# Kernel optimization log

Hardware: AMD Instinct MI355X
Metric: run time of the kernel (lower is better)

Reference implementation:

```python
import jax, jax.numpy as jnp
import numpy as np
from jax import lax

B, C_IN, C_OUT, H, W, K, PAD = 4, 64, 64, 96, 96, 3, 1
K2 = K * K


def setup_inputs() -> dict:
    key = jax.random.key(0)
    k1, k2, k3, k4, k5 = jax.random.split(key, 5)
    x = jax.random.normal(k1, (B, C_IN, H, W), jnp.float32)
    offset = jax.random.normal(k2, (B, 2 * K2, H, W), jnp.float32)
    weight = jax.random.normal(k3, (C_OUT, C_IN, K, K), jnp.float32) * 0.05
    mask_weight = jax.random.normal(k4, (K2, C_IN, K, K), jnp.float32) * 0.05
    mask_bias = jax.random.normal(k5, (K2,), jnp.float32) * 0.05
    return {"x": x, "offset": offset, "weight": weight,
            "mask_weight": mask_weight, "mask_bias": mask_bias}


def _deform_conv2d(x, offset, weight, mask):
    # torchvision ordering: per kernel tap k, offset[:, 2k] is dy, offset[:, 2k+1] is dx
    off_y = offset[:, 0::2]  # [B, K2, H, W]
    off_x = offset[:, 1::2]
    ky, kx = jnp.meshgrid(jnp.arange(K), jnp.arange(K), indexing="ij")
    ky = ky.reshape(K2).astype(x.dtype)
    kx = kx.reshape(K2).astype(x.dtype)
    hh = jnp.arange(H, dtype=x.dtype)
    ww = jnp.arange(W, dtype=x.dtype)
    base_y = hh[None, :, None] - PAD + ky[:, None, None]   # [K2, H, 1]
    base_x = ww[None, None, :] - PAD + kx[:, None, None]   # [K2, 1, W]
    py = base_y[None] + off_y                               # [B, K2, H, W]
    px = base_x[None] + off_x

    y0 = jnp.floor(py)
    x0 = jnp.floor(px)
    wy = py - y0   # bilinear weights
    wx = px - x0
    y0i = y0.astype(jnp.int32)
    x0i = x0.astype(jnp.int32)

    x_flat = x.reshape(B, C_IN, H * W)

    def gather(yy, xx):
        valid = (yy >= 0) & (yy < H) & (xx >= 0) & (xx < W)
        idx = jnp.clip(yy, 0, H - 1) * W + jnp.clip(xx, 0, W - 1)  # [B,K2,H,W]
        idx_f = idx.reshape(B, -1)
        v = jax.vmap(lambda xf, i: xf[:, i])(x_flat, idx_f)  # [B, C, K2*H*W]
        v = v.reshape(B, C_IN, K2, H, W)
        return v * valid[:, None].astype(v.dtype)

    v00 = gather(y0i, x0i)
    v01 = gather(y0i, x0i + 1)
    v10 = gather(y0i + 1, x0i)
    v11 = gather(y0i + 1, x0i + 1)

    wy_ = wy[:, None]  # [B,1,K2,H,W]
    wx_ = wx[:, None]
    sampled = (v00 * (1 - wy_) * (1 - wx_) + v01 * (1 - wy_) * wx_
               + v10 * wy_ * (1 - wx_) + v11 * wy_ * wx_)
    sampled = sampled * mask[:, None]  # modulate by sigmoid mask

    w2 = weight.reshape(C_OUT, C_IN, K2)
    return jnp.einsum("bckhw,ock->bohw", sampled, w2)


def reference(x, offset, weight, mask_weight, mask_bias):
    mask_logits = lax.conv_general_dilated(
        x, mask_weight, window_strides=(1, 1), padding=[(PAD, PAD), (PAD, PAD)],
        dimension_numbers=("NCHW", "OIHW", "NCHW"))
    mask = jax.nn.sigmoid(mask_logits + mask_bias[None, :, None, None])
    return _deform_conv2d(x, offset, weight, mask)
```

## Files before the change

kernel.cpp:

```cpp
#include <hip/hip_runtime.h>
#include <math.h>

#define BB 4
#define CI 64
#define CO 64
#define HH 96
#define WW 96
#define HW (HH*WW)
#define K2 9
#define PADC 1

#define TW 4
#define TH 4
#define TPXT (TW*TH)
#define TBX (WW/TW)
#define TBY (HH/TH)
#define NTILB (TBX*TBY)
#define NTILES (BB*NTILB)
#define GRID 512

#define WR 13
#define WC 16
#define SREC 72
#define NSLOT (WR*WC)
#define STASKS (WR*32*4)

typedef __attribute__((ext_vector_type(8))) short short8;
typedef __attribute__((ext_vector_type(4))) float float4v;

#define WF_USHORTS (18*64*32)
#define MWF_USHORTS (18*16*32)

__device__ __forceinline__ float bf2f(short s) {
    return __uint_as_float(((unsigned int)(unsigned short)s) << 16);
}
__device__ __forceinline__ short f2bf(float f) {
    unsigned int u = __float_as_uint(f);
    u = (u + 0x7fffu + ((u >> 16) & 1u)) >> 16;
    return (short)u;
}

__device__ __forceinline__ void unswz(int tt, int* b, int* ty, int* tx) {
    int g = tt & 7, r = tt >> 3;
    *b = g & 3;
    int tile = (g >> 2) * 288 + r;
    *ty = tile / TBX; *tx = tile % TBX;
}

__global__ __launch_bounds__(256) void pack_kernel(const float* __restrict__ wgt,
                                                   const float* __restrict__ mw,
                                                   unsigned short* __restrict__ Wf,
                                                   unsigned short* __restrict__ MWf) {
    int i = blockIdx.x * 256 + threadIdx.x;
    if (i < WF_USHORTS) {
        int frag = i >> 11;
        int o = (i >> 5) & 63;
        int tt = i & 31;
        int k = frag >> 1, cc = frag & 1;
        int c = cc * 32 + tt;
        Wf[i] = (unsigned short)f2bf(wgt[o * 576 + c * 9 + k]);
    } else if (i < WF_USHORTS + MWF_USHORTS) {
        int e = i - WF_USHORTS;
        int frag = e >> 9;
        int m = (e >> 5) & 15;
        int tt = e & 31;
        int q = frag >> 1, cc = frag & 1;
        int c = cc * 32 + tt;
        MWf[e] = (m < 9) ? (unsigned short)f2bf(mw[m * 576 + c * 9 + q]) : 0;
    }
}

struct SmemT {
    unsigned short win[NSLOT * SREC];
    float mred[2][2][K2][TPXT];
    int   idx[K2][4][TPXT];
    float w[K2][4][TPXT];
};

template<int KB, int KE>
__device__ __forceinline__ void run_tiles(SmemT& sm, int t, int wv, int ch, int tg,
                                          const float* __restrict__ x,
                                          const float* __restrict__ off,
                                          const float* __restrict__ mbias,
                                          const unsigned short* __restrict__ Wf,
                                          const unsigned short* __restrict__ MWf,
                                          float* __restrict__ out, int bid) {
    constexpr int NK = KE - KB;
    int lane = t & 63;
    int n = lane & 15, quad = lane >> 4;
    float* part = (float*)sm.win;

    short8 wA[NK][4];
    short8 mA[NK];
    #pragma unroll
    for (int kk = 0; kk < NK; kk++) {
        int k = KB + kk;
        const unsigned short* wp = Wf + (size_t)((k * 2 + ch) * 64) * 32 + quad * 8;
        #pragma unroll
        for (int s = 0; s < 4; s++)
            wA[kk][s] = *(const short8*)(wp + (s * 16 + n) * 32);
        mA[kk] = *(const short8*)(MWf + ((size_t)((k * 2 + ch) * 16 + n)) * 32 + quad * 8);
    }

    int ly = n >> 2, lx = n & 3;
    int cbase_us = ch * 32 + quad * 8;

    for (int tt = bid; tt < NTILES; tt += GRID) {
        int b, ty, tx; unswz(tt, &b, &ty, &tx);
        int h0 = ty * TH, w0 = tx * TW;
        int wr0 = h0 - 4, wc0 = w0 - 4;
        const float* xb = x + (size_t)b * CI * HW;
        int h = h0 + ly, wcc = w0 + lx;

        __syncthreads();

        for (int e = t; e < STASKS; e += 256) {
            int r = e >> 7;
            int chp = (e >> 2) & 31;
            int c4 = e & 3;
            int row = min(max(wr0 + r, 0), HH - 1);
            int c0c = wc0 + c4 * 4;
            const float* s0 = xb + (size_t)(2 * chp) * HW + row * WW;
            const float* s1 = s0 + HW;
            float v0[4], v1[4];
            if (c0c >= 0 && c0c + 3 < WW) {
                float4v a = *(const float4v*)(s0 + c0c);
                float4v bq = *(const float4v*)(s1 + c0c);
                v0[0]=a[0]; v0[1]=a[1]; v0[2]=a[2]; v0[3]=a[3];
                v1[0]=bq[0]; v1[1]=bq[1]; v1[2]=bq[2]; v1[3]=bq[3];
            } else {
                #pragma unroll
                for (int j = 0; j < 4; j++) {
                    int cc2 = min(max(c0c + j, 0), WW - 1);
                    v0[j] = s0[cc2]; v1[j] = s1[cc2];
                }
            }
            #pragma unroll
            for (int j = 0; j < 4; j++) {
                unsigned int pk = (unsigned short)f2bf(v0[j]) |
                                  ((unsigned int)(unsigned short)f2bf(v1[j]) << 16);
                *(unsigned int*)&sm.win[(r * WC + c4 * 4 + j) * SREC + 2 * chp] = pk;
            }
        }
        __syncthreads();

        {
            float4v macc = {0.f, 0.f, 0.f, 0.f};
            #pragma unroll
            for (int kk = 0; kk < NK; kk++) {
                int q = KB + kk;
                int hh = h + q / 3 - 1, ww2 = wcc + q % 3 - 1;
                bool valid = (hh >= 0) && (hh < HH) && (ww2 >= 0) && (ww2 < WW);
                short8 bfrag = {0, 0, 0, 0, 0, 0, 0, 0};
                if (valid) {
                    int slot = (hh - wr0) * WC + (ww2 - wc0);
                    bfrag = *(const short8*)&sm.win[slot * SREC + cbase_us];
                }
                macc = __builtin_amdgcn_mfma_f32_16x16x32_bf16(mA[kk], bfrag, macc, 0, 0, 0);
            }
            #pragma unroll
            for (int r = 0; r < 4; r++) {
                int row = quad * 4 + r;
                if (row < 9) sm.mred[ch][tg][row][n] = macc[r];
            }
        }
        __syncthreads();

        if (t < K2 * TPXT) {
            int k = t >> 4, pe = t & 15;
            int ph = h0 + (pe >> 2), pw = w0 + (pe & 3);
            int p = ph * WW + pw;
            float oy = off[((size_t)b * 2 * K2 + 2 * k) * HW + p];
            float ox = off[((size_t)b * 2 * K2 + 2 * k + 1) * HW + p];
            float s = sm.mred[0][0][k][pe] + sm.mred[0][1][k][pe] +
                      sm.mred[1][0][k][pe] + sm.mred[1][1][k][pe] + mbias[k];
            float m = 1.f / (1.f + expf(-s));
            float py  = (float)(ph - PADC + k / 3) + oy;
            float pxf = (float)(pw - PADC + k % 3) + ox;
            float y0f = floorf(py), x0f = floorf(pxf);
            float wy = py - y0f, wx = pxf - x0f;
            int y0 = (int)y0f, x0 = (int)x0f;
            int y1 = y0 + 1, x1 = x0 + 1;
            int y0c = min(max(y0, 0), HH - 1), y1c = min(max(y1, 0), HH - 1);
            int x0c = min(max(x0, 0), WW - 1), x1c = min(max(x1, 0), WW - 1);
            bool vy0 = (y0 >= 0) && (y0 < HH), vy1 = (y1 >= 0) && (y1 < HH);
            bool vx0 = (x0 >= 0) && (x0 < WW), vx1 = (x1 >= 0) && (x1 < WW);
            float w00 = (1.f - wy) * (1.f - wx) * m; if (!(vy0 && vx0)) w00 = 0.f;
            float w01 = (1.f - wy) * wx * m;         if (!(vy0 && vx1)) w01 = 0.f;
            float w10 = wy * (1.f - wx) * m;         if (!(vy1 && vx0)) w10 = 0.f;
            float w11 = wy * wx * m;                 if (!(vy1 && vx1)) w11 = 0.f;
            sm.idx[k][0][pe] = (y0c << 16) | x0c;
            sm.idx[k][1][pe] = (y0c << 16) | x1c;
            sm.idx[k][2][pe] = (y1c << 16) | x0c;
            sm.idx[k][3][pe] = (y1c << 16) | x1c;
            sm.w[k][0][pe] = w00; sm.w[k][1][pe] = w01;
            sm.w[k][2][pe] = w10; sm.w[k][3][pe] = w11;
        }
        __syncthreads();

        float4v acc0 = {0.f, 0.f, 0.f, 0.f};
        float4v acc1 = {0.f, 0.f, 0.f, 0.f};
        float4v acc2 = {0.f, 0.f, 0.f, 0.f};
        float4v acc3 = {0.f, 0.f, 0.f, 0.f};
        const float* xfb = xb + (size_t)(ch * 32 + quad * 8) * HW;

        #pragma unroll
        for (int kk = 0; kk < NK; kk++) {
            int k = KB + kk;
            short8 U[4];
            #pragma unroll
            for (int cor = 0; cor < 4; cor++) {
                int yx = sm.idx[k][cor][n];
                int yy = yx >> 16, xx = yx & 0xffff;
                int r = yy - wr0, c = xx - wc0;
                bool inw = ((unsigned)r < (unsigned)WR) && ((unsigned)c < (unsigned)WC);
                short8 u;
                if (inw) {
                    u = *(const short8*)&sm.win[(r * WC + c) * SREC + cbase_us];
                } else {
                    const float* fs = xfb + yy * WW + xx;
                    #pragma unroll
                    for (int j = 0; j < 8; j++) u[j] = f2bf(fs[(size_t)j * HW]);
                }
                U[cor] = u;
            }
            float w0 = sm.w[k][0][n], w1 = sm.w[k][1][n];
            float w2 = sm.w[k][2][n], w3 = sm.w[k][3][n];
            short8 bfrag;
            #pragma unroll
            for (int j = 0; j < 8; j++) {
                float v = bf2f(U[0][j]) * w0 + bf2f(U[1][j]) * w1 +
                          bf2f(U[2][j]) * w2 + bf2f(U[3][j]) * w3;
                bfrag[j] = f2bf(v);
            }
            acc0 = __builtin_amdgcn_mfma_f32_16x16x32_bf16(wA[kk][0], bfrag, acc0, 0, 0, 0);
            acc1 = __builtin_amdgcn_mfma_f32_16x16x32_bf16(wA[kk][1], bfrag, acc1, 0, 0, 0);
            acc2 = __builtin_amdgcn_mfma_f32_16x16x32_bf16(wA[kk][2], bfrag, acc2, 0, 0, 0);
            acc3 = __builtin_amdgcn_mfma_f32_16x16x32_bf16(wA[kk][3], bfrag, acc3, 0, 0, 0);
        }

        __syncthreads();
        if (wv != 0) {
            #pragma unroll
            for (int r = 0; r < 4; r++) {
                part[((wv - 1) * 16 + 0 * 4 + r) * 64 + lane] = acc0[r];
                part[((wv - 1) * 16 + 1 * 4 + r) * 64 + lane] = acc1[r];
                part[((wv - 1) * 16 + 2 * 4 + r) * 64 + lane] = acc2[r];
                part[((wv - 1) * 16 + 3 * 4 + r) * 64 + lane] = acc3[r];
            }
        }
        __syncthreads();
        if (wv == 0) {
            float* ob = out + (size_t)b * CO * HW + h * WW + wcc;
            #pragma unroll
            for (int r = 0; r < 4; r++) {
                int j0 = r, j1 = 4 + r, j2 = 8 + r, j3 = 12 + r;
                ob[(size_t)(0 * 16 + quad * 4 + r) * HW] = acc0[r] +
                    part[j0 * 64 + lane] + part[(16 + j0) * 64 + lane] + part[(32 + j0) * 64 + lane];
                ob[(size_t)(1 * 16 + quad * 4 + r) * HW] = acc1[r] +
                    part[j1 * 64 + lane] + part[(16 + j1) * 64 + lane] + part[(32 + j1) * 64 + lane];
                ob[(size_t)(2 * 16 + quad * 4 + r) * HW] = acc2[r] +
                    part[j2 * 64 + lane] + part[(16 + j2) * 64 + lane] + part[(32 + j2) * 64 + lane];
                ob[(size_t)(3 * 16 + quad * 4 + r) * HW] = acc3[r] +
                    part[j3 * 64 + lane] + part[(16 + j3) * 64 + lane] + part[(32 + j3) * 64 + lane];
            }
        }
    }
}

__global__ __launch_bounds__(256, 2) void fused_kernel(const float* __restrict__ x,
                                                       const float* __restrict__ off,
                                                       const float* __restrict__ mbias,
                                                       const unsigned short* __restrict__ Wf,
                                                       const unsigned short* __restrict__ MWf,
                                                       float* __restrict__ out) {
    __shared__ SmemT sm;
    int t = threadIdx.x;
    int wv = t >> 6;
    int ch = wv & 1, tg = wv >> 1;
    if (tg == 0)
        run_tiles<0, 5>(sm, t, wv, ch, tg, x, off, mbias, Wf, MWf, out, blockIdx.x);
    else
        run_tiles<5, 9>(sm, t, wv, ch, tg, x, off, mbias, Wf, MWf, out, blockIdx.x);
}

extern "C" void kernel_launch(void* const* d_in, const int* in_sizes, int n_in,
                              void* d_out, int out_size, void* d_ws, size_t ws_size,
                              hipStream_t stream) {
    const float* x   = (const float*)d_in[0];
    const float* off = (const float*)d_in[1];
    const float* wgt = (const float*)d_in[2];
    const float* mw  = (const float*)d_in[3];
    const float* mb  = (const float*)d_in[4];
    float* out = (float*)d_out;

    unsigned short* Wf  = (unsigned short*)d_ws;
    unsigned short* MWf = Wf + WF_USHORTS;

    hipLaunchKernelGGL(pack_kernel, dim3((WF_USHORTS + MWF_USHORTS + 255) / 256), dim3(256),
                       0, stream, wgt, mw, Wf, MWf);
    hipLaunchKernelGGL(fused_kernel, dim3(GRID), dim3(256), 0, stream,
                       x, off, mb, Wf, MWf, out);
}
```

Before: 115.2 us.

## Process vertical tile strips per block with a rolling ring buffer of input rows

Each block now walks a vertical strip of 4-5 tiles in one column instead of grid-striding over scattered tiles. It keeps a 16-row ring buffer of bf16 input rows in shared memory, so after the first tile only 4 new rows are staged rather than the full 13-row window. The record stride changes from 72 shorts to 35 dwords, read with dword loads, probably to cut LDS bank conflicts, and the partial-sum buffer gets its own storage. The cost is that the grid drops to 480 blocks with uneven strip lengths and each tile still serialises on staging, with less parallel slack.

```diff
diff --git a/kernel.cpp b/kernel.cpp
--- a/kernel.cpp
+++ b/kernel.cpp
@@ -12,18 +12,16 @@
 
 #define TW 4
 #define TH 4
-#define TPXT (TW*TH)
+#define TPXT 16
 #define TBX (WW/TW)
 #define TBY (HH/TH)
-#define NTILB (TBX*TBY)
-#define NTILES (BB*NTILB)
-#define GRID 512
-
-#define WR 13
+#define NTILES (BB*TBX*TBY)
+#define GRID 480
+
 #define WC 16
-#define SREC 72
-#define NSLOT (WR*WC)
-#define STASKS (WR*32*4)
+#define SREC 70
+#define RING 16
+#define NSLOT (RING*WC)
 
 typedef __attribute__((ext_vector_type(8))) short short8;
 typedef __attribute__((ext_vector_type(4))) float float4v;
@@ -38,13 +36,6 @@
     unsigned int u = __float_as_uint(f);
     u = (u + 0x7fffu + ((u >> 16) & 1u)) >> 16;
     return (short)u;
-}
-
-__device__ __forceinline__ void unswz(int tt, int* b, int* ty, int* tx) {
-    int g = tt & 7, r = tt >> 3;
-    *b = g & 3;
-    int tile = (g >> 2) * 288 + r;
-    *ty = tile / TBX; *tx = tile % TBX;
 }
 
 __global__ __launch_bounds__(256) void pack_kernel(const float* __restrict__ wgt,
@@ -75,10 +66,55 @@
     float mred[2][2][K2][TPXT];
     int   idx[K2][4][TPXT];
     float w[K2][4][TPXT];
+    float part[3][16][64];
 };
 
+__device__ __forceinline__ short8 ld_win(const unsigned int* w32, int dw) {
+    union { unsigned int u[4]; short8 s; } z;
+    z.u[0] = w32[dw + 0];
+    z.u[1] = w32[dw + 1];
+    z.u[2] = w32[dw + 2];
+    z.u[3] = w32[dw + 3];
+    return z.s;
+}
+
+__device__ __forceinline__ void stage_rows(unsigned int* w32, int t, int rs0, int nr,
+                                           int wc0, const float* __restrict__ xb) {
+    int ntask = nr * 128;
+    for (int e = t; e < ntask; e += 256) {
+        int ri = e >> 7;
+        int chp = (e >> 2) & 31;
+        int c4 = e & 3;
+        int label = rs0 + ri;
+        int row = min(max(label, 0), HH - 1);
+        int rslot = (label & 15) * WC;
+        int c0c = wc0 + c4 * 4;
+        const float* s0 = xb + (size_t)(2 * chp) * HW + row * WW;
+        const float* s1 = s0 + HW;
+        float v0[4], v1[4];
+        if (c0c >= 0 && c0c + 3 < WW) {
+            float4v a = *(const float4v*)(s0 + c0c);
+            float4v bq = *(const float4v*)(s1 + c0c);
+            v0[0]=a[0]; v0[1]=a[1]; v0[2]=a[2]; v0[3]=a[3];
+            v1[0]=bq[0]; v1[1]=bq[1]; v1[2]=bq[2]; v1[3]=bq[3];
+        } else {
+            #pragma unroll
+            for (int j = 0; j < 4; j++) {
+                int cc2 = min(max(c0c + j, 0), WW - 1);
+                v0[j] = s0[cc2]; v1[j] = s1[cc2];
+            }
+        }
+        #pragma unroll
+        for (int j = 0; j < 4; j++) {
+            unsigned int pk = (unsigned short)f2bf(v0[j]) |
+                              ((unsigned int)(unsigned short)f2bf(v1[j]) << 16);
+            w32[(rslot + c4 * 4 + j) * 35 + chp] = pk;
+        }
+    }
+}
+
 template<int KB, int KE>
-__device__ __forceinline__ void run_tiles(SmemT& sm, int t, int wv, int ch, int tg,
+__device__ __forceinline__ void run_strip(SmemT& sm, int t, int wv, int ch, int tg,
                                           const float* __restrict__ x,
                                           const float* __restrict__ off,
                                           const float* __restrict__ mbias,
@@ -88,7 +124,18 @@
     constexpr int NK = KE - KB;
     int lane = t & 63;
     int n = lane & 15, quad = lane >> 4;
-    float* part = (float*)sm.win;
+    unsigned int* w32 = (unsigned int*)sm.win;
+    const unsigned int* w32c = (const unsigned int*)sm.win;
+
+    int g = bid & 7, r = bid >> 3;
+    int b = g & 3, txh = g >> 2;
+    int col = r / 5, s = r % 5;
+    int tx = txh * 12 + col;
+    int ty0 = (s < 4) ? s * 5 : 20;
+    int len = (s < 4) ? 5 : 4;
+    int w0 = tx * TW;
+    int wc0 = w0 - 4;
+    const float* xb = x + (size_t)b * CI * HW;
 
     short8 wA[NK][4];
     short8 mA[NK];
@@ -97,51 +144,21 @@
         int k = KB + kk;
         const unsigned short* wp = Wf + (size_t)((k * 2 + ch) * 64) * 32 + quad * 8;
         #pragma unroll
-        for (int s = 0; s < 4; s++)
-            wA[kk][s] = *(const short8*)(wp + (s * 16 + n) * 32);
+        for (int ss = 0; ss < 4; ss++)
+            wA[kk][ss] = *(const short8*)(wp + (ss * 16 + n) * 32);
         mA[kk] = *(const short8*)(MWf + ((size_t)((k * 2 + ch) * 16 + n)) * 32 + quad * 8);
     }
 
     int ly = n >> 2, lx = n & 3;
-    int cbase_us = ch * 32 + quad * 8;
-
-    for (int tt = bid; tt < NTILES; tt += GRID) {
-        int b, ty, tx; unswz(tt, &b, &ty, &tx);
-        int h0 = ty * TH, w0 = tx * TW;
-        int wr0 = h0 - 4, wc0 = w0 - 4;
-        const float* xb = x + (size_t)b * CI * HW;
+    int cbase_dw = ch * 16 + quad * 4;
+
+    for (int j = 0; j < len; j++) {
+        int ty = ty0 + j;
+        int h0 = ty * TH;
         int h = h0 + ly, wcc = w0 + lx;
 
-        __syncthreads();
-
-        for (int e = t; e < STASKS; e += 256) {
-            int r = e >> 7;
-            int chp = (e >> 2) & 31;
-            int c4 = e & 3;
-            int row = min(max(wr0 + r, 0), HH - 1);
-            int c0c = wc0 + c4 * 4;
-            const float* s0 = xb + (size_t)(2 * chp) * HW + row * WW;
-            const float* s1 = s0 + HW;
-            float v0[4], v1[4];
-            if (c0c >= 0 && c0c + 3 < WW) {
-                float4v a = *(const float4v*)(s0 + c0c);
-                float4v bq = *(const float4v*)(s1 + c0c);
-                v0[0]=a[0]; v0[1]=a[1]; v0[2]=a[2]; v0[3]=a[3];
-                v1[0]=bq[0]; v1[1]=bq[1]; v1[2]=bq[2]; v1[3]=bq[3];
-            } else {
-                #pragma unroll
-                for (int j = 0; j < 4; j++) {
-                    int cc2 = min(max(c0c + j, 0), WW - 1);
-                    v0[j] = s0[cc2]; v1[j] = s1[cc2];
-                }
-            }
-            #pragma unroll
-            for (int j = 0; j < 4; j++) {
-                unsigned int pk = (unsigned short)f2bf(v0[j]) |
-                                  ((unsigned int)(unsigned short)f2bf(v1[j]) << 16);
-                *(unsigned int*)&sm.win[(r * WC + c4 * 4 + j) * SREC + 2 * chp] = pk;
-            }
-        }
+        if (j == 0) stage_rows(w32, t, h0 - 4, 13, wc0, xb);
+        else        stage_rows(w32, t, h0 + 5, 4, wc0, xb);
         __syncthreads();
 
         {
@@ -153,15 +170,15 @@
                 bool valid = (hh >= 0) && (hh < HH) && (ww2 >= 0) && (ww2 < WW);
                 short8 bfrag = {0, 0, 0, 0, 0, 0, 0, 0};
                 if (valid) {
-                    int slot = (hh - wr0) * WC + (ww2 - wc0);
-                    bfrag = *(const short8*)&sm.win[slot * SREC + cbase_us];
+                    int slot = (hh & 15) * WC + (ww2 - wc0);
+                    bfrag = ld_win(w32c, slot * 35 + cbase_dw);
                 }
                 macc = __builtin_amdgcn_mfma_f32_16x16x32_bf16(mA[kk], bfrag, macc, 0, 0, 0);
             }
             #pragma unroll
-            for (int r = 0; r < 4; r++) {
-                int row = quad * 4 + r;
-                if (row < 9) sm.mred[ch][tg][row][n] = macc[r];
+            for (int rr = 0; rr < 4; rr++) {
+                int row = quad * 4 + rr;
+                if (row < 9) sm.mred[ch][tg][row][n] = macc[rr];
             }
         }
         __syncthreads();
@@ -172,9 +189,9 @@
             int p = ph * WW + pw;
             float oy = off[((size_t)b * 2 * K2 + 2 * k) * HW + p];
             float ox = off[((size_t)b * 2 * K2 + 2 * k + 1) * HW + p];
-            float s = sm.mred[0][0][k][pe] + sm.mred[0][1][k][pe] +
-                      sm.mred[1][0][k][pe] + sm.mred[1][1][k][pe] + mbias[k];
-            float m = 1.f / (1.f + expf(-s));
+            float sl = sm.mred[0][0][k][pe] + sm.mred[0][1][k][pe] +
+                       sm.mred[1][0][k][pe] + sm.mred[1][1][k][pe] + mbias[k];
+            float m = 1.f / (1.f + expf(-sl));
             float py  = (float)(ph - PADC + k / 3) + oy;
             float pxf = (float)(pw - PADC + k % 3) + ox;
             float y0f = floorf(py), x0f = floorf(pxf);
@@ -212,26 +229,27 @@
             for (int cor = 0; cor < 4; cor++) {
                 int yx = sm.idx[k][cor][n];
                 int yy = yx >> 16, xx = yx & 0xffff;
-                int r = yy - wr0, c = xx - wc0;
-                bool inw = ((unsigned)r < (unsigned)WR) && ((unsigned)c < (unsigned)WC);
+                bool inw = (yy >= h0 - 4) && (yy <= h0 + 8) &&
+                           (xx >= wc0) && (xx <= wc0 + 15);
                 short8 u;
                 if (inw) {
-                    u = *(const short8*)&sm.win[(r * WC + c) * SREC + cbase_us];
+                    int slot = (yy & 15) * WC + (xx - wc0);
+                    u = ld_win(w32c, slot * 35 + cbase_dw);
                 } else {
                     const float* fs = xfb + yy * WW + xx;
                     #pragma unroll
-                    for (int j = 0; j < 8; j++) u[j] = f2bf(fs[(size_t)j * HW]);
+                    for (int jj = 0; jj < 8; jj++) u[jj] = f2bf(fs[(size_t)jj * HW]);
                 }
                 U[cor] = u;
             }
-            float w0 = sm.w[k][0][n], w1 = sm.w[k][1][n];
-            float w2 = sm.w[k][2][n], w3 = sm.w[k][3][n];
+            float w0v = sm.w[k][0][n], w1v = sm.w[k][1][n];
+            float w2v = sm.w[k][2][n], w3v = sm.w[k][3][n];
             short8 bfrag;
             #pragma unroll
-            for (int j = 0; j < 8; j++) {
-                float v = bf2f(U[0][j]) * w0 + bf2f(U[1][j]) * w1 +
-                          bf2f(U[2][j]) * w2 + bf2f(U[3][j]) * w3;
-                bfrag[j] = f2bf(v);
+            for (int jj = 0; jj < 8; jj++) {
+                float v = bf2f(U[0][jj]) * w0v + bf2f(U[1][jj]) * w1v +
+                          bf2f(U[2][jj]) * w2v + bf2f(U[3][jj]) * w3v;
+                bfrag[jj] = f2bf(v);
             }
             acc0 = __builtin_amdgcn_mfma_f32_16x16x32_bf16(wA[kk][0], bfrag, acc0, 0, 0, 0);
             acc1 = __builtin_amdgcn_mfma_f32_16x16x32_bf16(wA[kk][1], bfrag, acc1, 0, 0, 0);
@@ -239,32 +257,32 @@
             acc3 = __builtin_amdgcn_mfma_f32_16x16x32_bf16(wA[kk][3], bfrag, acc3, 0, 0, 0);
         }
 
-        __syncthreads();
         if (wv != 0) {
             #pragma unroll
-            for (int r = 0; r < 4; r++) {
-                part[((wv - 1) * 16 + 0 * 4 + r) * 64 + lane] = acc0[r];
-                part[((wv - 1) * 16 + 1 * 4 + r) * 64 + lane] = acc1[r];
-                part[((wv - 1) * 16 + 2 * 4 + r) * 64 + lane] = acc2[r];
-                part[((wv - 1) * 16 + 3 * 4 + r) * 64 + lane] = acc3[r];
+            for (int rr = 0; rr < 4; rr++) {
+                sm.part[wv - 1][0 * 4 + rr][lane] = acc0[rr];
+                sm.part[wv - 1][1 * 4 + rr][lane] = acc1[rr];
+                sm.part[wv - 1][2 * 4 + rr][lane] = acc2[rr];
+                sm.part[wv - 1][3 * 4 + rr][lane] = acc3[rr];
             }
         }
         __syncthreads();
         if (wv == 0) {
             float* ob = out + (size_t)b * CO * HW + h * WW + wcc;
             #pragma unroll
-            for (int r = 0; r < 4; r++) {
-                int j0 = r, j1 = 4 + r, j2 = 8 + r, j3 = 12 + r;
-                ob[(size_t)(0 * 16 + quad * 4 + r) * HW] = acc0[r] +
-                    part[j0 * 64 + lane] + part[(16 + j0) * 64 + lane] + part[(32 + j0) * 64 + lane];
-                ob[(size_t)(1 * 16 + quad * 4 + r) * HW] = acc1[r] +
-                    part[j1 * 64 + lane] + part[(16 + j1) * 64 + lane] + part[(32 + j1) * 64 + lane];
-                ob[(size_t)(2 * 16 + quad * 4 + r) * HW] = acc2[r] +
-                    part[j2 * 64 + lane] + part[(16 + j2) * 64 + lane] + part[(32 + j2) * 64 + lane];
-                ob[(size_t)(3 * 16 + quad * 4 + r) * HW] = acc3[r] +
-                    part[j3 * 64 + lane] + part[(16 + j3) * 64 + lane] + part[(32 + j3) * 64 + lane];
-            }
-        }
+            for (int rr = 0; rr < 4; rr++) {
+                int j0 = rr, j1 = 4 + rr, j2 = 8 + rr, j3 = 12 + rr;
+                ob[(size_t)(0 * 16 + quad * 4 + rr) * HW] = acc0[rr] +
+                    sm.part[0][j0][lane] + sm.part[1][j0][lane] + sm.part[2][j0][lane];
+                ob[(size_t)(1 * 16 + quad * 4 + rr) * HW] = acc1[rr] +
+                    sm.part[0][j1][lane] + sm.part[1][j1][lane] + sm.part[2][j1][lane];
+                ob[(size_t)(2 * 16 + quad * 4 + rr) * HW] = acc2[rr] +
+                    sm.part[0][j2][lane] + sm.part[1][j2][lane] + sm.part[2][j2][lane];
+                ob[(size_t)(3 * 16 + quad * 4 + rr) * HW] = acc3[rr] +
+                    sm.part[0][j3][lane] + sm.part[1][j3][lane] + sm.part[2][j3][lane];
+            }
+        }
+        __syncthreads();
     }
 }
 
@@ -279,9 +297,9 @@
     int wv = t >> 6;
     int ch = wv & 1, tg = wv >> 1;
     if (tg == 0)
-        run_tiles<0, 5>(sm, t, wv, ch, tg, x, off, mbias, Wf, MWf, out, blockIdx.x);
+        run_strip<0, 5>(sm, t, wv, ch, tg, x, off, mbias, Wf, MWf, out, blockIdx.x);
     else
-        run_tiles<5, 9>(sm, t, wv, ch, tg, x, off, mbias, Wf, MWf, out, blockIdx.x);
+        run_strip<5, 9>(sm, t, wv, ch, tg, x, off, mbias, Wf, MWf, out, blockIdx.x);
 }
 
 extern "C" void kernel_launch(void* const* d_in, const int* in_sizes, int n_in,
```

After: 106.8 us. -7.3%, faster.
